# Optimization experiments

Measured on AMD Instinct MI355X. Metric: run time of the kernel, lower is better.

The kernel has to match this reference:

```python
import jax, jax.numpy as jnp
import numpy as np

# Static problem structure (matches setup_inputs)
B, NPOLY, VPP, L = 32, 256, 64, 32
LAYERS = 3
PLEN = L * 2 ** LAYERS  # 256
LN_EPS = 1e-5


def _layernorm(h, g, b):
    mu = h.mean(-1, keepdims=True)
    var = ((h - mu) ** 2).mean(-1, keepdims=True)
    return g * (h - mu) / jnp.sqrt(var + LN_EPS) + b


def _forward(data, W0, b0, g0, beta0, W1, b1, g1, beta1, W2, b2, g2, beta2,
             Wq, bq, Wk, bk, Wv, bv):
    # row 0 holds agent polyline index in feature 0
    agent_id = data[:, 0, 0].astype(jnp.int32)  # [B]
    vecs = data[:, 1:, :]
    vecs = vecs.at[:, :, -1].set(0.0)  # zero out polyline-id feature (data[:,:,-1]=0)
    x = vecs.reshape(B, NPOLY, VPP, L)  # uniform polyline groups

    # SubGraph: 3 layers of (MLP -> maxpool aggregate -> concat), doubling width
    for (W, b, g, be) in ((W0, b0, g0, beta0), (W1, b1, g1, beta1), (W2, b2, g2, beta2)):
        h = jax.nn.relu(_layernorm(x @ W + b, g, be))  # [B,P,V,c]
        agg = h.max(axis=2, keepdims=True)             # [B,P,1,c]
        x = jnp.concatenate([h, jnp.broadcast_to(agg, h.shape)], axis=-1)  # [B,P,V,2c]
    P = x.max(axis=2)  # [B, NPOLY, PLEN] polyline features

    # Global graph: single-head attention with agent polyline as query
    q = P[jnp.arange(B), agent_id] @ Wq + bq          # [B, C]
    k = P @ Wk + bk                                    # [B, P, C]
    v = P @ Wv + bv
    scores = jnp.einsum('bc,bpc->bp', q, k) / jnp.sqrt(jnp.float32(PLEN))
    att = jax.nn.softmax(scores, axis=-1)
    return jnp.einsum('bp,bpc->bc', att, v)           # [B, PLEN]


def setup_inputs() -> dict:
    key = jax.random.key(0)
    ks = jax.random.split(key, 24)
    V = 1 + NPOLY * VPP
    data = jax.random.normal(ks[0], (B, V, L), dtype=jnp.float32)
    agent = jax.random.randint(ks[1], (B,), 0, NPOLY).astype(jnp.float32)
    data = data.at[:, 0, :].set(0.0).at[:, 0, 0].set(agent)
    pid = jnp.repeat(jnp.arange(NPOLY), VPP).astype(jnp.float32)
    data = data.at[:, 1:, -1].set(pid[None, :])

    inp = {'data': data}
    c = L
    for i in range(LAYERS):
        inp[f'W{i}'] = 0.02 * jax.random.normal(ks[2 + i], (c, c), dtype=jnp.float32)
        inp[f'b{i}'] = jnp.zeros((c,), jnp.float32)
        inp[f'g{i}'] = jnp.ones((c,), jnp.float32)
        inp[f'beta{i}'] = jnp.zeros((c,), jnp.float32)
        c *= 2
    C = PLEN
    for j, nm in enumerate(('q', 'k', 'v')):
        inp[f'W{nm}'] = 0.02 * jax.random.normal(ks[10 + j], (C, C), dtype=jnp.float32)
        inp[f'b{nm}'] = jnp.zeros((C,), jnp.float32)
    return inp


def reference(data, W0, b0, g0, beta0, W1, b1, g1, beta1, W2, b2, g2, beta2,
              Wq, bq, Wk, bk, Wv, bv):
    return _forward(data, W0, b0, g0, beta0, W1, b1, g1, beta1, W2, b2, g2, beta2,
                    Wq, bq, Wk, bk, Wv, bv)
```

## Files before the change

### kernel.cpp

```cpp
#include <hip/hip_runtime.h>

#define NPOLY 256
#define VPP   64
#define LCH   32
#define NV    (1 + NPOLY * VPP)
#define LN_EPS 1e-5f

typedef __bf16 bf16x8 __attribute__((ext_vector_type(8)));
typedef float  f32x4  __attribute__((ext_vector_type(4)));

union U4B8 { uint4 u; bf16x8 v; };

__device__ __forceinline__ unsigned packbf(float a, float b) {
    unsigned r;
    asm("v_cvt_pk_bf16_f32 %0, %1, %2" : "=v"(r) : "v"(a), "v"(b));
    return r;
}

__global__ void vn_prep1(const float* __restrict__ W0, const float* __restrict__ W1,
                         const float* __restrict__ W2,
                         const float* __restrict__ Wq, const float* __restrict__ Wk,
                         const float* __restrict__ Wv,
                         float* __restrict__ Wqf, float* __restrict__ Wkf,
                         float* __restrict__ Wvf, uint4* __restrict__ wpack)
{
    int t = blockIdx.x * 256 + threadIdx.x;
    if (t < 3 * 32768) {
        int which = t >> 15, r = t & 32767;
        const float* src = which == 0 ? Wq : which == 1 ? Wk : Wv;
        float*       dst = which == 0 ? Wqf : which == 1 ? Wkf : Wvf;
        dst[r] = src[r] + src[r + 128 * 256];
        return;
    }
    t -= 3 * 32768;
    if (t >= 22 * 64) return;
    int f = t >> 6, L = t & 63, q = L >> 4, m = L & 15;
    const float* src; int N, k0, col;
    if (f < 2)      { src = W0; N = 32;  k0 = q * 8;                 col = f * 16 + m; }
    else if (f < 6) { src = W1; N = 64;  k0 = q * 8;                 col = (f - 2) * 16 + m; }
    else { int g = f - 6; src = W2; N = 128; k0 = (g >> 3) * 32 + q * 8; col = (g & 7) * 16 + m; }
    float e[8];
    #pragma unroll
    for (int j = 0; j < 8; j++) e[j] = src[(k0 + j) * N + col];
    uint4 o;
    o.x = packbf(e[0], e[1]); o.y = packbf(e[2], e[3]);
    o.z = packbf(e[4], e[5]); o.w = packbf(e[6], e[7]);
    wpack[f * 64 + L] = o;
}

__global__ void vn_prep2(const float* __restrict__ Wqf, const float* __restrict__ Wkf,
                         const float* __restrict__ bq,
                         float* __restrict__ Mff, float* __restrict__ u0f)
{
    int t = blockIdx.x * 256 + threadIdx.x;
    if (t < 16384) {
        int i = t >> 7, j = t & 127;
        const float4* a = (const float4*)(Wqf + i * 256);
        const float4* b = (const float4*)(Wkf + j * 256);
        float s0 = 0.f, s1 = 0.f, s2 = 0.f, s3 = 0.f;
        #pragma unroll 4
        for (int c = 0; c < 64; c++) {
            float4 A = a[c], B = b[c];
            s0 = fmaf(A.x, B.x, s0); s1 = fmaf(A.y, B.y, s1);
            s2 = fmaf(A.z, B.z, s2); s3 = fmaf(A.w, B.w, s3);
        }
        Mff[i * 128 + j] = (s0 + s1) + (s2 + s3);
    } else if (t < 16512) {
        int j = t - 16384;
        const float4* a = (const float4*)bq;
        const float4* b = (const float4*)(Wkf + j * 256);
        float s0 = 0.f, s1 = 0.f, s2 = 0.f, s3 = 0.f;
        #pragma unroll 4
        for (int c = 0; c < 64; c++) {
            float4 A = a[c], B = b[c];
            s0 = fmaf(A.x, B.x, s0); s1 = fmaf(A.y, B.y, s1);
            s2 = fmaf(A.z, B.z, s2); s3 = fmaf(A.w, B.w, s3);
        }
        u0f[j] = (s0 + s1) + (s2 + s3);
    }
}

__global__ __launch_bounds__(256, 3) void vn_mlp(
    const float* __restrict__ data, const uint4* __restrict__ wpack,
    const float* __restrict__ b0, const float* __restrict__ g0, const float* __restrict__ be0,
    const float* __restrict__ W1, const float* __restrict__ b1,
    const float* __restrict__ g1, const float* __restrict__ be1,
    const float* __restrict__ W2, const float* __restrict__ b2,
    const float* __restrict__ g2, const float* __restrict__ be2,
    float* __restrict__ Ph)
{
    __shared__ __align__(16) unsigned short hbuf[64 * 72];
    __shared__ float partA[4][128];
    __shared__ float partB[4][128];

    const int tid = threadIdx.x;
    const int w = tid >> 6, L = tid & 63, q = L >> 4, m = L & 15;
    const int blk = blockIdx.x;
    const int bb = blk >> 8, pp = blk & 255;
    const int r0 = w * 16;

    const float* rowbase = data + ((size_t)bb * NV + 1 + (size_t)pp * VPP) * LCH;
    bf16x8 A0;
    {
        const float* rp = rowbase + (size_t)(r0 + m) * LCH + q * 8;
        float4 u = *(const float4*)rp;
        float4 v = *(const float4*)(rp + 4);
        if (q == 3) v.w = 0.f;
        U4B8 c;
        c.u.x = packbf(u.x, u.y); c.u.y = packbf(u.z, u.w);
        c.u.z = packbf(v.x, v.y); c.u.w = packbf(v.z, v.w);
        A0 = c.v;
    }
    f32x4 acc0[2];
    {
        U4B8 t0, t1; t0.u = wpack[0 * 64 + L]; t1.u = wpack[1 * 64 + L];
        float bca = b0[m], bcb = b0[16 + m];
        f32x4 a0 = { bca, bca, bca, bca };
        f32x4 a1 = { bcb, bcb, bcb, bcb };
        acc0[0] = __builtin_amdgcn_mfma_f32_16x16x32_bf16(A0, t0.v, a0, 0, 0, 0);
        acc0[1] = __builtin_amdgcn_mfma_f32_16x16x32_bf16(A0, t1.v, a1, 0, 0, 0);
    }
    {
        float g0c[2]  = { g0[m],  g0[16 + m]  };
        float be0c[2] = { be0[m], be0[16 + m] };
        float a0mx[2] = { 0.f, 0.f };
        #pragma unroll
        for (int reg = 0; reg < 4; reg++) {
            float x0 = acc0[0][reg], x1 = acc0[1][reg];
            float rs = x0 + x1, rq = x0 * x0 + x1 * x1;
            #pragma unroll
            for (int s = 1; s < 16; s <<= 1) { rs += __shfl_xor(rs, s, 64); rq += __shfl_xor(rq, s, 64); }
            float mu = rs * (1.f / 32.f);
            float var = rq * (1.f / 32.f) - mu * mu;
            float ri = rsqrtf(var + LN_EPS);
            #pragma unroll
            for (int ct = 0; ct < 2; ct++) {
                float v = fmaxf(fmaf(g0c[ct] * ri, acc0[ct][reg] - mu, be0c[ct]), 0.f);
                acc0[ct][reg] = v;
                a0mx[ct] = fmaxf(a0mx[ct], v);
            }
        }
        #pragma unroll
        for (int ct = 0; ct < 2; ct++) {
            float v = a0mx[ct];
            v = fmaxf(v, __shfl_xor(v, 16, 64));
            v = fmaxf(v, __shfl_xor(v, 32, 64));
            a0mx[ct] = v;
        }
        if (q == 0) { partA[w][m] = a0mx[0]; partA[w][16 + m] = a0mx[1]; }
    }
    #pragma unroll
    for (int reg = 0; reg < 4; reg++) {
        int row = r0 + q * 4 + reg;
        unsigned u = packbf(acc0[0][reg], acc0[1][reg]);
        hbuf[row * 72 + m]      = (unsigned short)u;
        hbuf[row * 72 + 16 + m] = (unsigned short)(u >> 16);
    }
    __syncthreads();

    {
        float p = 0.f;
        int j0 = w * 8;
        #pragma unroll
        for (int jj = 0; jj < 8; jj++) {
            int j = j0 + jj;
            float a = fmaxf(fmaxf(partA[0][j], partA[1][j]), fmaxf(partA[2][j], partA[3][j]));
            p = fmaf(a, W1[(32 + j) * 64 + L], p);
        }
        partB[w][L] = p;
    }
    __syncthreads();

    bf16x8 A1;
    { U4B8 c; c.u = *(const uint4*)(hbuf + (r0 + m) * 72 + q * 8); A1 = c.v; }
    f32x4 acc1[4];
    #pragma unroll
    for (int ct = 0; ct < 4; ct++) {
        U4B8 wv; wv.u = wpack[(2 + ct) * 64 + L];
        int n = ct * 16 + m;
        float au = b1[n] + ((partB[0][n] + partB[1][n]) + (partB[2][n] + partB[3][n]));
        f32x4 a = { au, au, au, au };
        acc1[ct] = __builtin_amdgcn_mfma_f32_16x16x32_bf16(A1, wv.v, a, 0, 0, 0);
    }
    {
        float g1c[4], be1c[4];
        #pragma unroll
        for (int ct = 0; ct < 4; ct++) { g1c[ct] = g1[ct * 16 + m]; be1c[ct] = be1[ct * 16 + m]; }
        float a1mx[4] = { 0.f, 0.f, 0.f, 0.f };
        #pragma unroll
        for (int reg = 0; reg < 4; reg++) {
            float rs = 0.f, rq = 0.f;
            #pragma unroll
            for (int ct = 0; ct < 4; ct++) { float x = acc1[ct][reg]; rs += x; rq += x * x; }
            #pragma unroll
            for (int s = 1; s < 16; s <<= 1) { rs += __shfl_xor(rs, s, 64); rq += __shfl_xor(rq, s, 64); }
            float mu = rs * (1.f / 64.f);
            float var = rq * (1.f / 64.f) - mu * mu;
            float ri = rsqrtf(var + LN_EPS);
            #pragma unroll
            for (int ct = 0; ct < 4; ct++) {
                float v = fmaxf(fmaf(g1c[ct] * ri, acc1[ct][reg] - mu, be1c[ct]), 0.f);
                acc1[ct][reg] = v;
                a1mx[ct] = fmaxf(a1mx[ct], v);
            }
        }
        #pragma unroll
        for (int ct = 0; ct < 4; ct++) {
            float v = a1mx[ct];
            v = fmaxf(v, __shfl_xor(v, 16, 64));
            v = fmaxf(v, __shfl_xor(v, 32, 64));
            a1mx[ct] = v;
        }
        if (q == 0) {
            #pragma unroll
            for (int ct = 0; ct < 4; ct++) partA[w][ct * 16 + m] = a1mx[ct];
        }
    }
    #pragma unroll
    for (int reg = 0; reg < 4; reg++) {
        int row = r0 + q * 4 + reg;
        unsigned ua = packbf(acc1[0][reg], acc1[1][reg]);
        unsigned ub = packbf(acc1[2][reg], acc1[3][reg]);
        hbuf[row * 72 + m]      = (unsigned short)ua;
        hbuf[row * 72 + 16 + m] = (unsigned short)(ua >> 16);
        hbuf[row * 72 + 32 + m] = (unsigned short)ub;
        hbuf[row * 72 + 48 + m] = (unsigned short)(ub >> 16);
    }
    __syncthreads();

    {
        float pa = 0.f, pb = 0.f;
        int j0 = w * 16;
        #pragma unroll
        for (int jj = 0; jj < 16; jj++) {
            int j = j0 + jj;
            float a = fmaxf(fmaxf(partA[0][j], partA[1][j]), fmaxf(partA[2][j], partA[3][j]));
            pa = fmaf(a, W2[(64 + j) * 128 + L],      pa);
            pb = fmaf(a, W2[(64 + j) * 128 + 64 + L], pb);
        }
        partB[w][L]      = pa;
        partB[w][64 + L] = pb;
    }
    __syncthreads();

    bf16x8 A2[2];
    #pragma unroll
    for (int ks = 0; ks < 2; ks++) {
        U4B8 c; c.u = *(const uint4*)(hbuf + (r0 + m) * 72 + ks * 32 + q * 8);
        A2[ks] = c.v;
    }
    f32x4 acc2[8];
    #pragma unroll
    for (int ct = 0; ct < 8; ct++) {
        U4B8 wa, wb;
        wa.u = wpack[(6 + ct) * 64 + L];
        wb.u = wpack[(14 + ct) * 64 + L];
        int n = ct * 16 + m;
        float au = b2[n] + ((partB[0][n] + partB[1][n]) + (partB[2][n] + partB[3][n]));
        f32x4 a = { au, au, au, au };
        a = __builtin_amdgcn_mfma_f32_16x16x32_bf16(A2[0], wa.v, a, 0, 0, 0);
        a = __builtin_amdgcn_mfma_f32_16x16x32_bf16(A2[1], wb.v, a, 0, 0, 0);
        acc2[ct] = a;
    }
    {
        float g2c[8], be2c[8];
        #pragma unroll
        for (int ct = 0; ct < 8; ct++) { g2c[ct] = g2[ct * 16 + m]; be2c[ct] = be2[ct * 16 + m]; }
        float m2[8] = { 0.f, 0.f, 0.f, 0.f, 0.f, 0.f, 0.f, 0.f };
        #pragma unroll
        for (int reg = 0; reg < 4; reg++) {
            float rs = 0.f, rq = 0.f;
            #pragma unroll
            for (int ct = 0; ct < 8; ct++) { float x = acc2[ct][reg]; rs += x; rq += x * x; }
            #pragma unroll
            for (int s = 1; s < 16; s <<= 1) { rs += __shfl_xor(rs, s, 64); rq += __shfl_xor(rq, s, 64); }
            float mu = rs * (1.f / 128.f);
            float var = rq * (1.f / 128.f) - mu * mu;
            float ri = rsqrtf(var + LN_EPS);
            #pragma unroll
            for (int ct = 0; ct < 8; ct++) {
                float v = fmaxf(fmaf(g2c[ct] * ri, acc2[ct][reg] - mu, be2c[ct]), 0.f);
                m2[ct] = fmaxf(m2[ct], v);
            }
        }
        #pragma unroll
        for (int ct = 0; ct < 8; ct++) {
            float v = m2[ct];
            v = fmaxf(v, __shfl_xor(v, 16, 64));
            v = fmaxf(v, __shfl_xor(v, 32, 64));
            m2[ct] = v;
        }
        if (q == 0) {
            #pragma unroll
            for (int ct = 0; ct < 8; ct++) partA[w][ct * 16 + m] = m2[ct];
        }
    }
    __syncthreads();

    if (tid < 128) {
        float v = fmaxf(fmaxf(partA[0][tid], partA[1][tid]),
                        fmaxf(partA[2][tid], partA[3][tid]));
        Ph[(size_t)blk * 128 + tid] = v;
    }
}

__global__ __launch_bounds__(256) void vn_attn(
    const float* __restrict__ data, const float* __restrict__ Ph,
    const float* __restrict__ Mff, const float* __restrict__ u0f,
    const float* __restrict__ Wvf, const float* __restrict__ bv,
    float* __restrict__ out)
{
    __shared__ __align__(16) float pah[128], tts[128], att[256], pb[128];
    __shared__ __align__(16) float part[256];
    __shared__ float red[8];
    const int b = blockIdx.x, tid = threadIdx.x, lane = tid & 63, wave = tid >> 6;
    const float* PhB = Ph + (size_t)b * NPOLY * 128;
    const int agent = (int)data[(size_t)b * NV * LCH];

    if (tid < 128) pah[tid] = PhB[(size_t)agent * 128 + tid];
    __syncthreads();

    {
        const int j = tid & 127, h = tid >> 7;
        const float* mc = Mff + (size_t)(h * 64) * 128 + j;
        const float* pv = pah + h * 64;
        float s0 = 0.f, s1 = 0.f, s2 = 0.f, s3 = 0.f;
        for (int i = 0; i < 64; i += 4) {
            s0 = fmaf(pv[i],     mc[(i)     * 128], s0);
            s1 = fmaf(pv[i + 1], mc[(i + 1) * 128], s1);
            s2 = fmaf(pv[i + 2], mc[(i + 2) * 128], s2);
            s3 = fmaf(pv[i + 3], mc[(i + 3) * 128], s3);
        }
        part[tid] = (s0 + s1) + (s2 + s3);
    }
    __syncthreads();
    if (tid < 128) tts[tid] = part[tid] + part[128 + tid] + u0f[tid];
    __syncthreads();

    float sv;
    {
        const float* pr = PhB + (size_t)tid * 128;
        float s0 = 0.f, s1 = 0.f, s2 = 0.f, s3 = 0.f;
        for (int j = 0; j < 128; j += 16) {
            float4 x0 = *(const float4*)(pr + j);
            float4 x1 = *(const float4*)(pr + j + 4);
            float4 x2 = *(const float4*)(pr + j + 8);
            float4 x3 = *(const float4*)(pr + j + 12);
            float4 t0 = *(const float4*)(tts + j);
            float4 t1 = *(const float4*)(tts + j + 4);
            float4 t2 = *(const float4*)(tts + j + 8);
            float4 t3 = *(const float4*)(tts + j + 12);
            s0 = fmaf(x0.w, t0.w, fmaf(x0.z, t0.z, fmaf(x0.y, t0.y, fmaf(x0.x, t0.x, s0))));
            s1 = fmaf(x1.w, t1.w, fmaf(x1.z, t1.z, fmaf(x1.y, t1.y, fmaf(x1.x, t1.x, s1))));
            s2 = fmaf(x2.w, t2.w, fmaf(x2.z, t2.z, fmaf(x2.y, t2.y, fmaf(x2.x, t2.x, s2))));
            s3 = fmaf(x3.w, t3.w, fmaf(x3.z, t3.z, fmaf(x3.y, t3.y, fmaf(x3.x, t3.x, s3))));
        }
        sv = ((s0 + s1) + (s2 + s3)) * 0.0625f;
    }
    float mx = sv;
    #pragma unroll
    for (int s = 1; s < 64; s <<= 1) mx = fmaxf(mx, __shfl_xor(mx, s, 64));
    if (lane == 0) red[wave] = mx;
    __syncthreads();
    mx = fmaxf(fmaxf(red[0], red[1]), fmaxf(red[2], red[3]));
    float e = expf(sv - mx);
    float sm = e;
    #pragma unroll
    for (int s = 1; s < 64; s <<= 1) sm += __shfl_xor(sm, s, 64);
    if (lane == 0) red[4 + wave] = sm;
    __syncthreads();
    const float tot = red[4] + red[5] + red[6] + red[7];
    att[tid] = e / tot;
    __syncthreads();

    {
        const int c = tid & 127, h = tid >> 7;
        const float* pp = PhB + (size_t)(h * 128) * 128 + c;
        const float* ap = att + h * 128;
        float s0 = 0.f, s1 = 0.f, s2 = 0.f, s3 = 0.f;
        for (int p = 0; p < 128; p += 4) {
            s0 = fmaf(ap[p],     pp[(p)     * 128], s0);
            s1 = fmaf(ap[p + 1], pp[(p + 1) * 128], s1);
            s2 = fmaf(ap[p + 2], pp[(p + 2) * 128], s2);
            s3 = fmaf(ap[p + 3], pp[(p + 3) * 128], s3);
        }
        part[tid] = (s0 + s1) + (s2 + s3);
    }
    __syncthreads();
    if (tid < 128) pb[tid] = part[tid] + part[128 + tid];
    __syncthreads();

    {
        const float* wv = Wvf + tid;
        float s0 = 0.f, s1 = 0.f, s2 = 0.f, s3 = 0.f;
        for (int j = 0; j < 128; j += 4) {
            s0 = fmaf(pb[j],     wv[(j)     * 256], s0);
            s1 = fmaf(pb[j + 1], wv[(j + 1) * 256], s1);
            s2 = fmaf(pb[j + 2], wv[(j + 2) * 256], s2);
            s3 = fmaf(pb[j + 3], wv[(j + 3) * 256], s3);
        }
        out[(size_t)b * 256 + tid] = bv[tid] + ((s0 + s1) + (s2 + s3));
    }
}

extern "C" void kernel_launch(void* const* d_in, const int* in_sizes, int n_in,
                              void* d_out, int out_size, void* d_ws, size_t ws_size,
                              hipStream_t stream)
{
    const float* data = (const float*)d_in[0];
    const float* W0 = (const float*)d_in[1];
    const float* b0 = (const float*)d_in[2];
    const float* g0 = (const float*)d_in[3];
    const float* be0= (const float*)d_in[4];
    const float* W1 = (const float*)d_in[5];
    const float* b1 = (const float*)d_in[6];
    const float* g1 = (const float*)d_in[7];
    const float* be1= (const float*)d_in[8];
    const float* W2 = (const float*)d_in[9];
    const float* b2 = (const float*)d_in[10];
    const float* g2 = (const float*)d_in[11];
    const float* be2= (const float*)d_in[12];
    const float* Wq = (const float*)d_in[13];
    const float* bq = (const float*)d_in[14];
    const float* Wk = (const float*)d_in[15];
    const float* bk = (const float*)d_in[16];
    const float* Wv = (const float*)d_in[17];
    const float* bv = (const float*)d_in[18];
    (void)bk;

    char* wsb = (char*)d_ws;
    float* Ph    = (float*)(wsb);
    float* Wqf   = (float*)(wsb + 4194304);
    float* Wkf   = (float*)(wsb + 4325376);
    float* Wvf   = (float*)(wsb + 4456448);
    float* Mff   = (float*)(wsb + 4587520);
    float* u0f   = (float*)(wsb + 4653056);
    uint4* wpack = (uint4*)(wsb + 4653568);

    vn_prep1<<<390, 256, 0, stream>>>(W0, W1, W2, Wq, Wk, Wv, Wqf, Wkf, Wvf, wpack);
    vn_prep2<<<65, 256, 0, stream>>>(Wqf, Wkf, bq, Mff, u0f);
    vn_mlp<<<32 * NPOLY, 256, 0, stream>>>(data, wpack,
                                           b0, g0, be0,
                                           W1, b1, g1, be1,
                                           W2, b2, g2, be2, Ph);
    vn_attn<<<32, 256, 0, stream>>>(data, Ph, Mff, u0f, Wvf, bv, (float*)d_out);
}
```

Before: 209.8 us.

## Merge prep kernels, use DPP row reductions, stage attention features in LDS

Merges the two weight-prep kernels into one launch by folding the Wq/Wk half-sums directly into the Mff and u0 dot products, so the Wqf and Wkf intermediates are no longer written. Replaces the LayerNorm shuffle-xor reductions in the MLP kernel with DPP row operations over 16 lanes. The attention kernel now copies each batch's 256x128 polyline feature block into about 129 KB of padded dynamic shared memory and reads both the score and weighted-sum passes from it. The trade-offs are one very large LDS allocation per block in a 32-block kernel and redundant Wq/Wk loads inside the Mff loop.

```diff
diff --git a/kernel.cpp b/kernel.cpp
--- a/kernel.cpp
+++ b/kernel.cpp
@@ -17,64 +17,77 @@
     return r;
 }
 
-__global__ void vn_prep1(const float* __restrict__ W0, const float* __restrict__ W1,
-                         const float* __restrict__ W2,
-                         const float* __restrict__ Wq, const float* __restrict__ Wk,
-                         const float* __restrict__ Wv,
-                         float* __restrict__ Wqf, float* __restrict__ Wkf,
-                         float* __restrict__ Wvf, uint4* __restrict__ wpack)
+#define DPPF(x, ctrl) __int_as_float(__builtin_amdgcn_update_dpp(0, __float_as_int(x), (ctrl), 0xF, 0xF, true))
+
+__device__ __forceinline__ float red16sum(float x) {
+    x += DPPF(x, 0xB1);
+    x += DPPF(x, 0x4E);
+    x += DPPF(x, 0x141);
+    x += DPPF(x, 0x140);
+    return x;
+}
+
+__global__ void vn_prep(const float* __restrict__ W0, const float* __restrict__ W1,
+                        const float* __restrict__ W2,
+                        const float* __restrict__ Wq, const float* __restrict__ Wk,
+                        const float* __restrict__ Wv, const float* __restrict__ bq,
+                        float* __restrict__ Wvf, uint4* __restrict__ wpack,
+                        float* __restrict__ Mff, float* __restrict__ u0f)
 {
     int t = blockIdx.x * 256 + threadIdx.x;
-    if (t < 3 * 32768) {
-        int which = t >> 15, r = t & 32767;
-        const float* src = which == 0 ? Wq : which == 1 ? Wk : Wv;
-        float*       dst = which == 0 ? Wqf : which == 1 ? Wkf : Wvf;
-        dst[r] = src[r] + src[r + 128 * 256];
+    if (t < 32768) {
+        Wvf[t] = Wv[t] + Wv[t + 128 * 256];
         return;
     }
-    t -= 3 * 32768;
-    if (t >= 22 * 64) return;
-    int f = t >> 6, L = t & 63, q = L >> 4, m = L & 15;
-    const float* src; int N, k0, col;
-    if (f < 2)      { src = W0; N = 32;  k0 = q * 8;                 col = f * 16 + m; }
-    else if (f < 6) { src = W1; N = 64;  k0 = q * 8;                 col = (f - 2) * 16 + m; }
-    else { int g = f - 6; src = W2; N = 128; k0 = (g >> 3) * 32 + q * 8; col = (g & 7) * 16 + m; }
-    float e[8];
-    #pragma unroll
-    for (int j = 0; j < 8; j++) e[j] = src[(k0 + j) * N + col];
-    uint4 o;
-    o.x = packbf(e[0], e[1]); o.y = packbf(e[2], e[3]);
-    o.z = packbf(e[4], e[5]); o.w = packbf(e[6], e[7]);
-    wpack[f * 64 + L] = o;
-}
-
-__global__ void vn_prep2(const float* __restrict__ Wqf, const float* __restrict__ Wkf,
-                         const float* __restrict__ bq,
-                         float* __restrict__ Mff, float* __restrict__ u0f)
-{
-    int t = blockIdx.x * 256 + threadIdx.x;
+    t -= 32768;
+    if (t < 22 * 64) {
+        int f = t >> 6, L = t & 63, q = L >> 4, m = L & 15;
+        const float* src; int N, k0, col;
+        if (f < 2)      { src = W0; N = 32;  k0 = q * 8;                 col = f * 16 + m; }
+        else if (f < 6) { src = W1; N = 64;  k0 = q * 8;                 col = (f - 2) * 16 + m; }
+        else { int g = f - 6; src = W2; N = 128; k0 = (g >> 3) * 32 + q * 8; col = (g & 7) * 16 + m; }
+        float e[8];
+        #pragma unroll
+        for (int j = 0; j < 8; j++) e[j] = src[(k0 + j) * N + col];
+        uint4 o;
+        o.x = packbf(e[0], e[1]); o.y = packbf(e[2], e[3]);
+        o.z = packbf(e[4], e[5]); o.w = packbf(e[6], e[7]);
+        wpack[f * 64 + L] = o;
+        return;
+    }
+    t -= 22 * 64;
     if (t < 16384) {
         int i = t >> 7, j = t & 127;
-        const float4* a = (const float4*)(Wqf + i * 256);
-        const float4* b = (const float4*)(Wkf + j * 256);
+        const float4* q0 = (const float4*)(Wq + (size_t)i * 256);
+        const float4* q1 = (const float4*)(Wq + (size_t)(i + 128) * 256);
+        const float4* k0 = (const float4*)(Wk + (size_t)j * 256);
+        const float4* k1 = (const float4*)(Wk + (size_t)(j + 128) * 256);
         float s0 = 0.f, s1 = 0.f, s2 = 0.f, s3 = 0.f;
         #pragma unroll 4
         for (int c = 0; c < 64; c++) {
-            float4 A = a[c], B = b[c];
-            s0 = fmaf(A.x, B.x, s0); s1 = fmaf(A.y, B.y, s1);
-            s2 = fmaf(A.z, B.z, s2); s3 = fmaf(A.w, B.w, s3);
+            float4 A0 = q0[c], A1 = q1[c], B0 = k0[c], B1 = k1[c];
+            s0 = fmaf(A0.x + A1.x, B0.x + B1.x, s0);
+            s1 = fmaf(A0.y + A1.y, B0.y + B1.y, s1);
+            s2 = fmaf(A0.z + A1.z, B0.z + B1.z, s2);
+            s3 = fmaf(A0.w + A1.w, B0.w + B1.w, s3);
         }
         Mff[i * 128 + j] = (s0 + s1) + (s2 + s3);
-    } else if (t < 16512) {
-        int j = t - 16384;
-        const float4* a = (const float4*)bq;
-        const float4* b = (const float4*)(Wkf + j * 256);
+        return;
+    }
+    t -= 16384;
+    if (t < 128) {
+        int j = t;
+        const float4* a  = (const float4*)bq;
+        const float4* k0 = (const float4*)(Wk + (size_t)j * 256);
+        const float4* k1 = (const float4*)(Wk + (size_t)(j + 128) * 256);
         float s0 = 0.f, s1 = 0.f, s2 = 0.f, s3 = 0.f;
         #pragma unroll 4
         for (int c = 0; c < 64; c++) {
-            float4 A = a[c], B = b[c];
-            s0 = fmaf(A.x, B.x, s0); s1 = fmaf(A.y, B.y, s1);
-            s2 = fmaf(A.z, B.z, s2); s3 = fmaf(A.w, B.w, s3);
+            float4 A = a[c]; float4 B0 = k0[c], B1 = k1[c];
+            s0 = fmaf(A.x, B0.x + B1.x, s0);
+            s1 = fmaf(A.y, B0.y + B1.y, s1);
+            s2 = fmaf(A.z, B0.z + B1.z, s2);
+            s3 = fmaf(A.w, B0.w + B1.w, s3);
         }
         u0f[j] = (s0 + s1) + (s2 + s3);
     }
@@ -127,9 +140,8 @@
         #pragma unroll
         for (int reg = 0; reg < 4; reg++) {
             float x0 = acc0[0][reg], x1 = acc0[1][reg];
-            float rs = x0 + x1, rq = x0 * x0 + x1 * x1;
-            #pragma unroll
-            for (int s = 1; s < 16; s <<= 1) { rs += __shfl_xor(rs, s, 64); rq += __shfl_xor(rq, s, 64); }
+            float rs = red16sum(x0 + x1);
+            float rq = red16sum(x0 * x0 + x1 * x1);
             float mu = rs * (1.f / 32.f);
             float var = rq * (1.f / 32.f) - mu * mu;
             float ri = rsqrtf(var + LN_EPS);
@@ -191,9 +203,9 @@
         for (int reg = 0; reg < 4; reg++) {
             float rs = 0.f, rq = 0.f;
             #pragma unroll
-            for (int ct = 0; ct < 4; ct++) { float x = acc1[ct][reg]; rs += x; rq += x * x; }
-            #pragma unroll
-            for (int s = 1; s < 16; s <<= 1) { rs += __shfl_xor(rs, s, 64); rq += __shfl_xor(rq, s, 64); }
+            for (int ct = 0; ct < 4; ct++) { float x = acc1[ct][reg]; rs += x; rq = fmaf(x, x, rq); }
+            rs = red16sum(rs);
+            rq = red16sum(rq);
             float mu = rs * (1.f / 64.f);
             float var = rq * (1.f / 64.f) - mu * mu;
             float ri = rsqrtf(var + LN_EPS);
@@ -271,9 +283,9 @@
         for (int reg = 0; reg < 4; reg++) {
             float rs = 0.f, rq = 0.f;
             #pragma unroll
-            for (int ct = 0; ct < 8; ct++) { float x = acc2[ct][reg]; rs += x; rq += x * x; }
-            #pragma unroll
-            for (int s = 1; s < 16; s <<= 1) { rs += __shfl_xor(rs, s, 64); rq += __shfl_xor(rq, s, 64); }
+            for (int ct = 0; ct < 8; ct++) { float x = acc2[ct][reg]; rs += x; rq = fmaf(x, x, rq); }
+            rs = red16sum(rs);
+            rq = red16sum(rq);
             float mu = rs * (1.f / 128.f);
             float var = rq * (1.f / 128.f) - mu * mu;
             float ri = rsqrtf(var + LN_EPS);
@@ -310,6 +322,7 @@
     const float* __restrict__ Wvf, const float* __restrict__ bv,
     float* __restrict__ out)
 {
+    extern __shared__ float shPh[];
     __shared__ __align__(16) float pah[128], tts[128], att[256], pb[128];
     __shared__ __align__(16) float part[256];
     __shared__ float red[8];
@@ -318,6 +331,18 @@
     const int agent = (int)data[(size_t)b * NV * LCH];
 
     if (tid < 128) pah[tid] = PhB[(size_t)agent * 128 + tid];
+    {
+        const float4* src = (const float4*)PhB;
+        #pragma unroll
+        for (int it = 0; it < 32; it++) {
+            int idx4 = it * 256 + tid;
+            float4 v = src[idx4];
+            int lin = idx4 * 4;
+            int p = lin >> 7, c = lin & 127;
+            float* dst = shPh + p * 129 + c;
+            dst[0] = v.x; dst[1] = v.y; dst[2] = v.z; dst[3] = v.w;
+        }
+    }
     __syncthreads();
 
     {
@@ -325,6 +350,7 @@
         const float* mc = Mff + (size_t)(h * 64) * 128 + j;
         const float* pv = pah + h * 64;
         float s0 = 0.f, s1 = 0.f, s2 = 0.f, s3 = 0.f;
+        #pragma unroll
         for (int i = 0; i < 64; i += 4) {
             s0 = fmaf(pv[i],     mc[(i)     * 128], s0);
             s1 = fmaf(pv[i + 1], mc[(i + 1) * 128], s1);
@@ -339,21 +365,14 @@
 
     float sv;
     {
-        const float* pr = PhB + (size_t)tid * 128;
-        float s0 = 0.f, s1 = 0.f, s2 = 0.f, s3 = 0.f;
-        for (int j = 0; j < 128; j += 16) {
-            float4 x0 = *(const float4*)(pr + j);
-            float4 x1 = *(const float4*)(pr + j + 4);
-            float4 x2 = *(const float4*)(pr + j + 8);
-            float4 x3 = *(const float4*)(pr + j + 12);
-            float4 t0 = *(const float4*)(tts + j);
-            float4 t1 = *(const float4*)(tts + j + 4);
-            float4 t2 = *(const float4*)(tts + j + 8);
-            float4 t3 = *(const float4*)(tts + j + 12);
-            s0 = fmaf(x0.w, t0.w, fmaf(x0.z, t0.z, fmaf(x0.y, t0.y, fmaf(x0.x, t0.x, s0))));
-            s1 = fmaf(x1.w, t1.w, fmaf(x1.z, t1.z, fmaf(x1.y, t1.y, fmaf(x1.x, t1.x, s1))));
-            s2 = fmaf(x2.w, t2.w, fmaf(x2.z, t2.z, fmaf(x2.y, t2.y, fmaf(x2.x, t2.x, s2))));
-            s3 = fmaf(x3.w, t3.w, fmaf(x3.z, t3.z, fmaf(x3.y, t3.y, fmaf(x3.x, t3.x, s3))));
+        const float* prl = shPh + tid * 129;
+        float s0 = 0.f, s1 = 0.f, s2 = 0.f, s3 = 0.f;
+        #pragma unroll
+        for (int j = 0; j < 128; j += 4) {
+            s0 = fmaf(prl[j],     tts[j],     s0);
+            s1 = fmaf(prl[j + 1], tts[j + 1], s1);
+            s2 = fmaf(prl[j + 2], tts[j + 2], s2);
+            s3 = fmaf(prl[j + 3], tts[j + 3], s3);
         }
         sv = ((s0 + s1) + (s2 + s3)) * 0.0625f;
     }
@@ -375,14 +394,15 @@
 
     {
         const int c = tid & 127, h = tid >> 7;
-        const float* pp = PhB + (size_t)(h * 128) * 128 + c;
         const float* ap = att + h * 128;
-        float s0 = 0.f, s1 = 0.f, s2 = 0.f, s3 = 0.f;
+        const float* pp = shPh + (size_t)(h * 128) * 129 + c;
+        float s0 = 0.f, s1 = 0.f, s2 = 0.f, s3 = 0.f;
+        #pragma unroll
         for (int p = 0; p < 128; p += 4) {
-            s0 = fmaf(ap[p],     pp[(p)     * 128], s0);
-            s1 = fmaf(ap[p + 1], pp[(p + 1) * 128], s1);
-            s2 = fmaf(ap[p + 2], pp[(p + 2) * 128], s2);
-            s3 = fmaf(ap[p + 3], pp[(p + 3) * 128], s3);
+            s0 = fmaf(ap[p],     pp[(p)     * 129], s0);
+            s1 = fmaf(ap[p + 1], pp[(p + 1) * 129], s1);
+            s2 = fmaf(ap[p + 2], pp[(p + 2) * 129], s2);
+            s3 = fmaf(ap[p + 3], pp[(p + 3) * 129], s3);
         }
         part[tid] = (s0 + s1) + (s2 + s3);
     }
@@ -393,6 +413,7 @@
     {
         const float* wv = Wvf + tid;
         float s0 = 0.f, s1 = 0.f, s2 = 0.f, s3 = 0.f;
+        #pragma unroll
         for (int j = 0; j < 128; j += 4) {
             s0 = fmaf(pb[j],     wv[(j)     * 256], s0);
             s1 = fmaf(pb[j + 1], wv[(j + 1) * 256], s1);
@@ -430,18 +451,22 @@
 
     char* wsb = (char*)d_ws;
     float* Ph    = (float*)(wsb);
-    float* Wqf   = (float*)(wsb + 4194304);
-    float* Wkf   = (float*)(wsb + 4325376);
     float* Wvf   = (float*)(wsb + 4456448);
     float* Mff   = (float*)(wsb + 4587520);
     float* u0f   = (float*)(wsb + 4653056);
     uint4* wpack = (uint4*)(wsb + 4653568);
 
-    vn_prep1<<<390, 256, 0, stream>>>(W0, W1, W2, Wq, Wk, Wv, Wqf, Wkf, Wvf, wpack);
-    vn_prep2<<<65, 256, 0, stream>>>(Wqf, Wkf, bq, Mff, u0f);
+    static int attn_attr_set = 0;
+    if (!attn_attr_set) {
+        hipFuncSetAttribute((const void*)vn_attn,
+                            hipFuncAttributeMaxDynamicSharedMemorySize, 132096);
+        attn_attr_set = 1;
+    }
+
+    vn_prep<<<198, 256, 0, stream>>>(W0, W1, W2, Wq, Wk, Wv, bq, Wvf, wpack, Mff, u0f);
     vn_mlp<<<32 * NPOLY, 256, 0, stream>>>(data, wpack,
                                            b0, g0, be0,
                                            W1, b1, g1, be1,
                                            W2, b2, g2, be2, Ph);
-    vn_attn<<<32, 256, 0, stream>>>(data, Ph, Mff, u0f, Wvf, bv, (float*)d_out);
-}
+    vn_attn<<<32, 256, 132096, stream>>>(data, Ph, Mff, u0f, Wvf, bv, (float*)d_out);
+}
```

Measured after the change: 204.7 us. 1.02x faster.
